# Optimization experiments

Hardware: AMD Instinct MI355X
Metric: run time of the kernel (lower is better)

## Reference

```python
import jax, jax.numpy as jnp
import numpy as np

B, T, V = 4096, 32, 256          # batch, decode steps, vocab
E, CE, H, L, NH = 768, 64, 256, 2, 4  # eword_dim, char_emb_dim, hidden, gru layers, heads
HD = H // NH                      # head dim
BOS, PAD = 1, 0


def _gru_cell(x, h, w_ih, w_hh, b_ih, b_hh):
    # PyTorch GRUCell math: gates ordered (r, z, n)
    gi = x @ w_ih.T + b_ih
    gh = h @ w_hh.T + b_hh
    ir, iz, inn = jnp.split(gi, 3, axis=-1)
    hr, hz, hn = jnp.split(gh, 3, axis=-1)
    r = jax.nn.sigmoid(ir + hr)
    z = jax.nn.sigmoid(iz + hz)
    n = jnp.tanh(inn + r * hn)
    return (1.0 - z) * n + z * h


def setup_inputs() -> dict:
    key = jax.random.key(0)
    ks = jax.random.split(key, 24)
    s = 0.02
    p = lambda k, shp: (jax.random.normal(k, shp, jnp.float32) * s)
    return {
        "eword": jax.random.normal(ks[0], (B, E), jnp.float32),
        "target_ids": jax.random.randint(ks[1], (B, T), 0, V),
        # params
        "char_emb": p(ks[2], (V, CE)).at[PAD].set(0.0),
        "eword_proj_w": p(ks[3], (H, E)), "eword_proj_b": p(ks[4], (H,)),
        "gru_w_ih0": p(ks[5], (3 * H, CE + E)), "gru_w_hh0": p(ks[6], (3 * H, H)),
        "gru_b_ih0": p(ks[7], (3 * H,)), "gru_b_hh0": p(ks[8], (3 * H,)),
        "gru_w_ih1": p(ks[9], (3 * H, H)), "gru_w_hh1": p(ks[10], (3 * H, H)),
        "gru_b_ih1": p(ks[11], (3 * H,)), "gru_b_hh1": p(ks[12], (3 * H,)),
        "attn_in_w": p(ks[13], (3 * H, H)), "attn_in_b": p(ks[14], (3 * H,)),
        "attn_out_w": p(ks[15], (H, H)), "attn_out_b": p(ks[16], (H,)),
        "key_w": p(ks[17], (H, E)), "key_b": p(ks[18], (H,)),
        "val_w": p(ks[19], (H, E)), "val_b": p(ks[20], (H,)),
        "proj_w": p(ks[21], (V, H)), "proj_b": p(ks[22], (V,)),
    }


def reference(eword, target_ids, char_emb, eword_proj_w, eword_proj_b,
              gru_w_ih0, gru_w_hh0, gru_b_ih0, gru_b_hh0,
              gru_w_ih1, gru_w_hh1, gru_b_ih1, gru_b_hh1,
              attn_in_w, attn_in_b, attn_out_w, attn_out_b,
              key_w, key_b, val_w, val_b, proj_w, proj_b):
    batch = eword.shape[0]
    # init hidden: tanh(Linear(eword)) broadcast across layers
    h0 = jnp.tanh(eword @ eword_proj_w.T + eword_proj_b)
    # pre-projected key/value (seq len 1), then MHA in-proj for k,v (static)
    wq, wk, wv = jnp.split(attn_in_w, 3, axis=0)
    bq, bk, bv = jnp.split(attn_in_b, 3)
    ek = (eword @ key_w.T + key_b) @ wk.T + bk        # (B, H)
    ev = (eword @ val_w.T + val_b) @ wv.T + bv        # (B, H)
    kh = ek.reshape(batch, NH, HD)                     # (B, NH, HD)
    vh = ev.reshape(batch, NH, HD)
    scale = 1.0 / np.sqrt(HD).astype(np.float32)

    # teacher forcing: input at step t is BOS for t=0, else target_ids[:, t-1]
    in_ids = jnp.concatenate(
        [jnp.full((batch, 1), BOS, target_ids.dtype), target_ids[:, :-1]], axis=1)

    def step(carry, ids):
        h_l0, h_l1 = carry
        ce = char_emb[ids] * (ids != PAD)[:, None].astype(char_emb.dtype)
        x = jnp.concatenate([ce, eword], axis=-1)     # (B, CE+E)
        h_l0 = _gru_cell(x, h_l0, gru_w_ih0, gru_w_hh0, gru_b_ih0, gru_b_hh0)
        h_l1 = _gru_cell(h_l0, h_l1, gru_w_ih1, gru_w_hh1, gru_b_ih1, gru_b_hh1)
        # single-query cross-attention over a length-1 key/value
        q = (h_l1 @ wq.T + bq).reshape(batch, NH, HD)
        score = jnp.sum(q * kh, axis=-1, keepdims=True) * scale  # (B, NH, 1)
        w = jax.nn.softmax(score, axis=-1)            # ones (len-1 softmax)
        attn = (w * vh).reshape(batch, H)
        attn_out = attn @ attn_out_w.T + attn_out_b
        out = h_l1 + attn_out
        logits = out @ proj_w.T + proj_b              # (B, V)
        return (h_l0, h_l1), logits

    _, logits_t = jax.lax.scan(step, (h0, h0), in_ids.T)  # (T, B, V)
    return jnp.transpose(logits_t, (1, 0, 2))              # (B, T, V)
```

## Files before the change

### kernel.cpp

```cpp
#include <hip/hip_runtime.h>


typedef __bf16 bf16;
typedef __attribute__((ext_vector_type(8))) __bf16 bf16x8;
typedef __attribute__((ext_vector_type(4))) __bf16 bf16x4;
typedef __attribute__((ext_vector_type(4))) float fx4;

#define MFMA16(a, b, c) __builtin_amdgcn_mfma_f32_16x16x32_bf16(a, b, c, 0, 0, 0)

__device__ __forceinline__ float sigm(float x) { return 1.0f / (1.0f + expf(-x)); }

__device__ __forceinline__ bf16x8 cvt8(const float* __restrict__ p) {
    float4 u = ((const float4*)p)[0];
    float4 v = ((const float4*)p)[1];
    bf16x8 r;
    r[0] = (bf16)u.x; r[1] = (bf16)u.y; r[2] = (bf16)u.z; r[3] = (bf16)u.w;
    r[4] = (bf16)v.x; r[5] = (bf16)v.y; r[6] = (bf16)v.z; r[7] = (bf16)v.w;
    return r;
}

__device__ __forceinline__ bf16x8 addcvt8(bf16x8 h, const float* __restrict__ p) {
    float4 u = ((const float4*)p)[0];
    float4 v = ((const float4*)p)[1];
    bf16x8 r;
    r[0] = (bf16)((float)h[0] + u.x); r[1] = (bf16)((float)h[1] + u.y);
    r[2] = (bf16)((float)h[2] + u.z); r[3] = (bf16)((float)h[3] + u.w);
    r[4] = (bf16)((float)h[4] + v.x); r[5] = (bf16)((float)h[5] + v.y);
    r[6] = (bf16)((float)h[6] + v.z); r[7] = (bf16)((float)h[7] + v.w);
    return r;
}

__global__ void f2b(const float* __restrict__ s, bf16* __restrict__ d, int n) {
    int i = (blockIdx.x * 256 + threadIdx.x) * 4;
    if (i >= n) return;
    float4 v = *(const float4*)(s + i);
    bf16x4 o;
    o[0] = (bf16)v.x; o[1] = (bf16)v.y; o[2] = (bf16)v.z; o[3] = (bf16)v.w;
    *(bf16x4*)(d + i) = o;
}

__global__ __launch_bounds__(256, 4) void gemm_bt(
    const float* __restrict__ A, int lda,
    const float* __restrict__ W, int ldw,
    const float* __restrict__ bias,
    float* __restrict__ out, int ldo, int act_tanh, int K)
{
    const int tid  = threadIdx.x;
    const int wid  = tid >> 6;
    const int lane = tid & 63;
    const int quad = lane >> 4;
    const int l16  = lane & 15;
    const int m0   = blockIdx.x * 32;
    const int n0   = blockIdx.y * 256 + wid * 64;

    fx4 acc[4][2];
#pragma unroll
    for (int j = 0; j < 4; ++j) {
        acc[j][0] = fx4{0.f, 0.f, 0.f, 0.f};
        acc[j][1] = fx4{0.f, 0.f, 0.f, 0.f};
    }

    const float* a0p = A + (size_t)(m0 + l16) * lda + quad * 8;
    const float* a1p = A + (size_t)(m0 + 16 + l16) * lda + quad * 8;

    for (int k0 = 0; k0 < K; k0 += 32) {
        bf16x8 a0 = cvt8(a0p + k0);
        bf16x8 a1 = cvt8(a1p + k0);
#pragma unroll
        for (int j = 0; j < 4; ++j) {
            bf16x8 b = cvt8(W + (size_t)(n0 + j * 16 + l16) * ldw + k0 + quad * 8);
            acc[j][0] = MFMA16(a0, b, acc[j][0]);
            acc[j][1] = MFMA16(a1, b, acc[j][1]);
        }
    }

#pragma unroll
    for (int j = 0; j < 4; ++j) {
        int n = n0 + j * 16 + l16;
        float bv = bias ? bias[n] : 0.0f;
#pragma unroll
        for (int rt = 0; rt < 2; ++rt)
#pragma unroll
            for (int r = 0; r < 4; ++r) {
                int m = m0 + rt * 16 + quad * 4 + r;
                float v = acc[j][rt][r] + bv;
                if (act_tanh) v = tanhf(v);
                out[(size_t)m * ldo + n] = v;
            }
    }
}

__global__ __launch_bounds__(1024, 4) void decoder_loop(
    const int*   __restrict__ tgt,
    const float* __restrict__ h0i,
    const float* __restrict__ gword,
    const float* __restrict__ cproj,
    const bf16*  __restrict__ w_hh0, const float* __restrict__ b_hh0,
    const bf16*  __restrict__ w_ih1, const float* __restrict__ b_ih1,
    const bf16*  __restrict__ w_hh1, const float* __restrict__ b_hh1,
    bf16* __restrict__ h1all)
{
    __shared__ __align__(16) bf16 hb0[2][16][264];
    __shared__ __align__(16) bf16 hb1[2][16][264];

    const int tid  = threadIdx.x;
    const int wid  = tid >> 6;
    const int lane = tid & 63;
    const int quad = lane >> 4;
    const int l16  = lane & 15;
    const int row0 = blockIdx.x * 16;
    const int col  = wid * 16 + l16;
    const int rw   = quad * 4;

    float h0m[4], h1m[4], cg[3][4];
    float bh0[3], bi1[3], bh1[3];
#pragma unroll
    for (int g = 0; g < 3; ++g) {
        bh0[g] = b_hh0[g * 256 + col];
        bi1[g] = b_ih1[g * 256 + col];
        bh1[g] = b_hh1[g * 256 + col];
    }
#pragma unroll
    for (int r = 0; r < 4; ++r) {
        int row = row0 + rw + r;
        float v = h0i[(size_t)row * 256 + col];
        h0m[r] = v; h1m[r] = v;
        bf16 bv = (bf16)v;
        hb0[0][rw + r][col] = bv; hb1[0][rw + r][col] = bv;
#pragma unroll
        for (int g = 0; g < 3; ++g)
            cg[g][r] = cproj[(size_t)768 + g * 256 + col]
                     + gword[(size_t)row * 768 + g * 256 + col];
    }

    const char* Wp0 = (const char*)w_hh0;
    const char* Wp1 = (const char*)w_ih1;
    const char* Wp2 = (const char*)w_hh1;
    int woff[3];
#pragma unroll
    for (int g = 0; g < 3; ++g)
        woff[g] = ((g * 256 + col) * 256 + quad * 8) * 2;

    __syncthreads();

    for (int t = 0; t < 32; ++t) {
        const int p = t & 1, q = p ^ 1;

        int nid[4];
#pragma unroll
        for (int r = 0; r < 4; ++r)
            nid[r] = tgt[(row0 + rw + r) * 32 + t];

        fx4 g0[3], g1[3];
#pragma unroll
        for (int g = 0; g < 3; ++g) {
            g0[g] = fx4{0.f, 0.f, 0.f, 0.f};
            g1[g] = fx4{0.f, 0.f, 0.f, 0.f};
        }
        bf16x8 av[2], cv[2], wb0[2], wb2[2];
        av[0] = *(const bf16x8*)&hb0[p][l16][quad * 8];
        cv[0] = *(const bf16x8*)&hb1[p][l16][quad * 8];
        av[1] = *(const bf16x8*)&hb0[p][l16][32 + quad * 8];
        cv[1] = *(const bf16x8*)&hb1[p][l16][32 + quad * 8];
        wb0[0] = *(const bf16x8*)(Wp0 + woff[0]);
        wb2[0] = *(const bf16x8*)(Wp2 + woff[0]);
        wb0[1] = *(const bf16x8*)(Wp0 + woff[1]);
        wb2[1] = *(const bf16x8*)(Wp2 + woff[1]);
#pragma unroll
        for (int kk = 0; kk < 8; ++kk) {
            bf16x8 au = av[kk & 1], cu = cv[kk & 1];
            if (kk < 6) {
                av[kk & 1] = *(const bf16x8*)&hb0[p][l16][(kk + 2) * 32 + quad * 8];
                cv[kk & 1] = *(const bf16x8*)&hb1[p][l16][(kk + 2) * 32 + quad * 8];
            }
#pragma unroll
            for (int g = 0; g < 3; ++g) {
                const int s = kk * 3 + g;
                bf16x8 b0 = wb0[s & 1], b2 = wb2[s & 1];
                if (s + 2 < 24) {
                    const int g2 = (s + 2) % 3, k2 = (s + 2) / 3;
                    wb0[s & 1] = *(const bf16x8*)(Wp0 + woff[g2] + k2 * 64);
                    wb2[s & 1] = *(const bf16x8*)(Wp2 + woff[g2] + k2 * 64);
                }
                g0[g] = MFMA16(au, b0, g0[g]);
                g1[g] = MFMA16(cu, b2, g1[g]);
            }
        }
#pragma unroll
        for (int r = 0; r < 4; ++r) {
            float rr = sigm(cg[0][r] + g0[0][r] + bh0[0]);
            float zz = sigm(cg[1][r] + g0[1][r] + bh0[1]);
            float nn = tanhf(cg[2][r] + rr * (g0[2][r] + bh0[2]));
            h0m[r] = (1.0f - zz) * nn + zz * h0m[r];
            hb0[q][rw + r][col] = (bf16)h0m[r];
        }
        __syncthreads();

        float cgn[3][4];
#pragma unroll
        for (int g = 0; g < 3; ++g)
#pragma unroll
            for (int r = 0; r < 4; ++r)
                cgn[g][r] = cproj[(size_t)nid[r] * 768 + g * 256 + col]
                          + gword[(size_t)(row0 + rw + r) * 768 + g * 256 + col];

        fx4 gi[3];
#pragma unroll
        for (int g = 0; g < 3; ++g) gi[g] = fx4{0.f, 0.f, 0.f, 0.f};
        bf16x8 bv2[2], wb1[2];
        bv2[0] = *(const bf16x8*)&hb0[q][l16][quad * 8];
        bv2[1] = *(const bf16x8*)&hb0[q][l16][32 + quad * 8];
        wb1[0] = *(const bf16x8*)(Wp1 + woff[0]);
        wb1[1] = *(const bf16x8*)(Wp1 + woff[1]);
#pragma unroll
        for (int kk = 0; kk < 8; ++kk) {
            bf16x8 au = bv2[kk & 1];
            if (kk < 6)
                bv2[kk & 1] = *(const bf16x8*)&hb0[q][l16][(kk + 2) * 32 + quad * 8];
#pragma unroll
            for (int g = 0; g < 3; ++g) {
                const int s = kk * 3 + g;
                bf16x8 b = wb1[s & 1];
                if (s + 2 < 24) {
                    const int g2 = (s + 2) % 3, k2 = (s + 2) / 3;
                    wb1[s & 1] = *(const bf16x8*)(Wp1 + woff[g2] + k2 * 64);
                }
                gi[g] = MFMA16(au, b, gi[g]);
            }
        }
#pragma unroll
        for (int r = 0; r < 4; ++r) {
            float rr = sigm(gi[0][r] + bi1[0] + g1[0][r] + bh1[0]);
            float zz = sigm(gi[1][r] + bi1[1] + g1[1][r] + bh1[1]);
            float nn = tanhf(gi[2][r] + bi1[2] + rr * (g1[2][r] + bh1[2]));
            h1m[r] = (1.0f - zz) * nn + zz * h1m[r];
            bf16 hv = (bf16)h1m[r];
            hb1[q][rw + r][col] = hv;
            __builtin_nontemporal_store(
                hv, &h1all[((size_t)(row0 + rw + r) * 32 + t) * 256 + col]);
        }
#pragma unroll
        for (int g = 0; g < 3; ++g)
#pragma unroll
            for (int r = 0; r < 4; ++r) cg[g][r] = cgn[g][r];

        __syncthreads();
    }
}

__global__ __launch_bounds__(256, 4) void logits_final(
    const bf16*  __restrict__ h1,
    const float* __restrict__ a2,
    const bf16*  __restrict__ pw,
    const float* __restrict__ pb,
    float* __restrict__ out)
{
    const int tid  = threadIdx.x;
    const int wid  = tid >> 6;
    const int lane = tid & 63;
    const int quad = lane >> 4;
    const int l16  = lane & 15;
    const int m0   = blockIdx.x * 32;
    const int n0   = wid * 64;
    const int b    = m0 >> 5;

    fx4 acc[4][2];
#pragma unroll
    for (int j = 0; j < 4; ++j) {
        acc[j][0] = fx4{0.f, 0.f, 0.f, 0.f};
        acc[j][1] = fx4{0.f, 0.f, 0.f, 0.f};
    }

    for (int k0 = 0; k0 < 256; k0 += 32) {
        bf16x8 h0 = *(const bf16x8*)(h1 + (size_t)(m0 + l16) * 256 + k0 + quad * 8);
        bf16x8 h1v = *(const bf16x8*)(h1 + (size_t)(m0 + 16 + l16) * 256 + k0 + quad * 8);
        const float* ap = a2 + (size_t)b * 256 + k0 + quad * 8;
        bf16x8 a0 = addcvt8(h0, ap);
        bf16x8 a1 = addcvt8(h1v, ap);
#pragma unroll
        for (int j = 0; j < 4; ++j) {
            bf16x8 bb = *(const bf16x8*)(pw + (size_t)(n0 + j * 16 + l16) * 256 + k0 + quad * 8);
            acc[j][0] = MFMA16(a0, bb, acc[j][0]);
            acc[j][1] = MFMA16(a1, bb, acc[j][1]);
        }
    }

#pragma unroll
    for (int j = 0; j < 4; ++j) {
        int n = n0 + j * 16 + l16;
        float bv = pb[n];
#pragma unroll
        for (int rt = 0; rt < 2; ++rt)
#pragma unroll
            for (int r = 0; r < 4; ++r) {
                int m = m0 + rt * 16 + quad * 4 + r;
                out[(size_t)m * 256 + n] = acc[j][rt][r] + bv;
            }
    }
}

extern "C" void kernel_launch(void* const* d_in, const int* in_sizes, int n_in,
                              void* d_out, int out_size, void* d_ws, size_t ws_size,
                              hipStream_t stream)
{
    const float* eword      = (const float*)d_in[0];
    const int*   tgt        = (const int*)  d_in[1];
    const float* char_emb   = (const float*)d_in[2];
    const float* ew_w       = (const float*)d_in[3];
    const float* ew_b       = (const float*)d_in[4];
    const float* w_ih0      = (const float*)d_in[5];
    const float* w_hh0      = (const float*)d_in[6];
    const float* b_ih0      = (const float*)d_in[7];
    const float* b_hh0      = (const float*)d_in[8];
    const float* w_ih1      = (const float*)d_in[9];
    const float* w_hh1      = (const float*)d_in[10];
    const float* b_ih1      = (const float*)d_in[11];
    const float* b_hh1      = (const float*)d_in[12];
    const float* attn_in_w  = (const float*)d_in[13];
    const float* attn_in_b  = (const float*)d_in[14];
    const float* attn_out_w = (const float*)d_in[15];
    const float* attn_out_b = (const float*)d_in[16];
    const float* val_w      = (const float*)d_in[19];
    const float* val_b      = (const float*)d_in[20];
    const float* proj_w     = (const float*)d_in[21];
    const float* proj_b     = (const float*)d_in[22];

    char* ws = (char*)d_ws;
    float* h0i   = (float*)ws;  ws += (size_t)4096 * 256 * 4;
    float* gwrd  = (float*)ws;  ws += (size_t)4096 * 768 * 4;
    float* cproj = (float*)ws;  ws += (size_t)256  * 768 * 4;
    float* a2    = (float*)ws;  ws += (size_t)4096 * 256 * 4;
    float* buf1  = (float*)ws;  ws += (size_t)4096 * 256 * 4;
    float* buf2  = (float*)ws;  ws += (size_t)4096 * 256 * 4;
    bf16*  wbhh0 = (bf16*)ws;   ws += (size_t)768 * 256 * 2;
    bf16*  wbih1 = (bf16*)ws;   ws += (size_t)768 * 256 * 2;
    bf16*  wbhh1 = (bf16*)ws;   ws += (size_t)768 * 256 * 2;
    bf16*  wbprj = (bf16*)ws;   ws += (size_t)256 * 256 * 2;
    bf16*  h1all = (bf16*)ws;   ws += (size_t)4096 * 32 * 256 * 2;

    dim3 blk(256);
    f2b<<<dim3(192), blk, 0, stream>>>(w_hh0, wbhh0, 768 * 256);
    f2b<<<dim3(192), blk, 0, stream>>>(w_ih1, wbih1, 768 * 256);
    f2b<<<dim3(192), blk, 0, stream>>>(w_hh1, wbhh1, 768 * 256);
    f2b<<<dim3(64),  blk, 0, stream>>>(proj_w, wbprj, 256 * 256);

    gemm_bt<<<dim3(128, 1), blk, 0, stream>>>(eword, 768, ew_w, 768, ew_b, h0i, 256, 1, 768);
    gemm_bt<<<dim3(128, 3), blk, 0, stream>>>(eword, 768, w_ih0 + 64, 832, b_ih0, gwrd, 768, 0, 768);
    gemm_bt<<<dim3(8, 3),   blk, 0, stream>>>(char_emb, 64, w_ih0, 832, nullptr, cproj, 768, 0, 64);
    gemm_bt<<<dim3(128, 1), blk, 0, stream>>>(eword, 768, val_w, 768, val_b, buf1, 256, 0, 768);
    gemm_bt<<<dim3(128, 1), blk, 0, stream>>>(buf1, 256, attn_in_w + 512 * 256, 256, attn_in_b + 512, buf2, 256, 0, 256);
    gemm_bt<<<dim3(128, 1), blk, 0, stream>>>(buf2, 256, attn_out_w, 256, attn_out_b, a2, 256, 0, 256);

    decoder_loop<<<dim3(256), dim3(1024), 0, stream>>>(
        tgt, h0i, gwrd, cproj,
        wbhh0, b_hh0, wbih1, b_ih1, wbhh1, b_hh1, h1all);

    logits_final<<<dim3(4096), blk, 0, stream>>>(h1all, a2, wbprj, proj_b, (float*)d_out);
}
```

Before: 2.263 ms.

## Pack GRU weights into per-wave MFMA fragment layout for coalesced loads

Adds a packing kernel that reorders the three bf16 GRU weight matrices so each wave's B-fragments for all gates and K-chunks are laid out contiguously. Each 16-lane group then reads 512 contiguous bytes per fragment instead of rows strided by 512 bytes. The decoder loop switches to a one-ahead prefetch of all three gate fragments per K-chunk and moves the target-id load to after the barrier. Register pressure may rise because six weight fragments are held in flight at once.

```diff
diff --git a/kernel.cpp b/kernel.cpp
--- a/kernel.cpp
+++ b/kernel.cpp
@@ -37,6 +37,17 @@
     bf16x4 o;
     o[0] = (bf16)v.x; o[1] = (bf16)v.y; o[2] = (bf16)v.z; o[3] = (bf16)v.w;
     *(bf16x4*)(d + i) = o;
+}
+
+__global__ void wpack(const float* __restrict__ src, bf16* __restrict__ dst) {
+    int gid = blockIdx.x * 256 + threadIdx.x;
+    if (gid >= 768 * 32) return;
+    int gc = gid >> 5, piece = gid & 31;
+    int g = gc >> 8, rem = gc & 255, w = rem >> 4, l16 = rem & 15;
+    int c = piece >> 2, quad = piece & 3;
+    bf16x8 v = cvt8(src + (size_t)gc * 256 + piece * 8);
+    size_t d = (size_t)w * 12288 + (size_t)(c * 3 + g) * 512 + l16 * 32 + quad * 8;
+    *(bf16x8*)(dst + d) = v;
 }
 
 __global__ __launch_bounds__(256, 4) void gemm_bt(
@@ -95,9 +106,9 @@
     const float* __restrict__ h0i,
     const float* __restrict__ gword,
     const float* __restrict__ cproj,
-    const bf16*  __restrict__ w_hh0, const float* __restrict__ b_hh0,
-    const bf16*  __restrict__ w_ih1, const float* __restrict__ b_ih1,
-    const bf16*  __restrict__ w_hh1, const float* __restrict__ b_hh1,
+    const bf16*  __restrict__ w_hh0p, const float* __restrict__ b_hh0,
+    const bf16*  __restrict__ w_ih1p, const float* __restrict__ b_ih1,
+    const bf16*  __restrict__ w_hh1p, const float* __restrict__ b_hh1,
     bf16* __restrict__ h1all)
 {
     __shared__ __align__(16) bf16 hb0[2][16][264];
@@ -112,6 +123,10 @@
     const int col  = wid * 16 + l16;
     const int rw   = quad * 4;
 
+    const bf16* pW0 = w_hh0p + (size_t)wid * 12288 + l16 * 32 + quad * 8;
+    const bf16* pW1 = w_ih1p + (size_t)wid * 12288 + l16 * 32 + quad * 8;
+    const bf16* pW2 = w_hh1p + (size_t)wid * 12288 + l16 * 32 + quad * 8;
+
     float h0m[4], h1m[4], cg[3][4];
     float bh0[3], bi1[3], bh1[3];
 #pragma unroll
@@ -133,23 +148,10 @@
                      + gword[(size_t)row * 768 + g * 256 + col];
     }
 
-    const char* Wp0 = (const char*)w_hh0;
-    const char* Wp1 = (const char*)w_ih1;
-    const char* Wp2 = (const char*)w_hh1;
-    int woff[3];
-#pragma unroll
-    for (int g = 0; g < 3; ++g)
-        woff[g] = ((g * 256 + col) * 256 + quad * 8) * 2;
-
     __syncthreads();
 
     for (int t = 0; t < 32; ++t) {
         const int p = t & 1, q = p ^ 1;
-
-        int nid[4];
-#pragma unroll
-        for (int r = 0; r < 4; ++r)
-            nid[r] = tgt[(row0 + rw + r) * 32 + t];
 
         fx4 g0[3], g1[3];
 #pragma unroll
@@ -157,33 +159,35 @@
             g0[g] = fx4{0.f, 0.f, 0.f, 0.f};
             g1[g] = fx4{0.f, 0.f, 0.f, 0.f};
         }
-        bf16x8 av[2], cv[2], wb0[2], wb2[2];
-        av[0] = *(const bf16x8*)&hb0[p][l16][quad * 8];
-        cv[0] = *(const bf16x8*)&hb1[p][l16][quad * 8];
-        av[1] = *(const bf16x8*)&hb0[p][l16][32 + quad * 8];
-        cv[1] = *(const bf16x8*)&hb1[p][l16][32 + quad * 8];
-        wb0[0] = *(const bf16x8*)(Wp0 + woff[0]);
-        wb2[0] = *(const bf16x8*)(Wp2 + woff[0]);
-        wb0[1] = *(const bf16x8*)(Wp0 + woff[1]);
-        wb2[1] = *(const bf16x8*)(Wp2 + woff[1]);
+        bf16x8 a_c, c_c, w0[3], w2[3];
+        a_c = *(const bf16x8*)&hb0[p][l16][quad * 8];
+        c_c = *(const bf16x8*)&hb1[p][l16][quad * 8];
+#pragma unroll
+        for (int g = 0; g < 3; ++g) {
+            w0[g] = *(const bf16x8*)(pW0 + g * 512);
+            w2[g] = *(const bf16x8*)(pW2 + g * 512);
+        }
 #pragma unroll
         for (int kk = 0; kk < 8; ++kk) {
-            bf16x8 au = av[kk & 1], cu = cv[kk & 1];
-            if (kk < 6) {
-                av[kk & 1] = *(const bf16x8*)&hb0[p][l16][(kk + 2) * 32 + quad * 8];
-                cv[kk & 1] = *(const bf16x8*)&hb1[p][l16][(kk + 2) * 32 + quad * 8];
+            bf16x8 a_n, c_n, w0n[3], w2n[3];
+            if (kk < 7) {
+                a_n = *(const bf16x8*)&hb0[p][l16][(kk + 1) * 32 + quad * 8];
+                c_n = *(const bf16x8*)&hb1[p][l16][(kk + 1) * 32 + quad * 8];
+#pragma unroll
+                for (int g = 0; g < 3; ++g) {
+                    w0n[g] = *(const bf16x8*)(pW0 + ((kk + 1) * 3 + g) * 512);
+                    w2n[g] = *(const bf16x8*)(pW2 + ((kk + 1) * 3 + g) * 512);
+                }
             }
 #pragma unroll
             for (int g = 0; g < 3; ++g) {
-                const int s = kk * 3 + g;
-                bf16x8 b0 = wb0[s & 1], b2 = wb2[s & 1];
-                if (s + 2 < 24) {
-                    const int g2 = (s + 2) % 3, k2 = (s + 2) / 3;
-                    wb0[s & 1] = *(const bf16x8*)(Wp0 + woff[g2] + k2 * 64);
-                    wb2[s & 1] = *(const bf16x8*)(Wp2 + woff[g2] + k2 * 64);
-                }
-                g0[g] = MFMA16(au, b0, g0[g]);
-                g1[g] = MFMA16(cu, b2, g1[g]);
+                g0[g] = MFMA16(a_c, w0[g], g0[g]);
+                g1[g] = MFMA16(c_c, w2[g], g1[g]);
+            }
+            if (kk < 7) {
+                a_c = a_n; c_c = c_n;
+#pragma unroll
+                for (int g = 0; g < 3; ++g) { w0[g] = w0n[g]; w2[g] = w2n[g]; }
             }
         }
 #pragma unroll
@@ -196,6 +200,10 @@
         }
         __syncthreads();
 
+        int nid[4];
+#pragma unroll
+        for (int r = 0; r < 4; ++r)
+            nid[r] = tgt[(row0 + rw + r) * 32 + t];
         float cgn[3][4];
 #pragma unroll
         for (int g = 0; g < 3; ++g)
@@ -207,25 +215,27 @@
         fx4 gi[3];
 #pragma unroll
         for (int g = 0; g < 3; ++g) gi[g] = fx4{0.f, 0.f, 0.f, 0.f};
-        bf16x8 bv2[2], wb1[2];
-        bv2[0] = *(const bf16x8*)&hb0[q][l16][quad * 8];
-        bv2[1] = *(const bf16x8*)&hb0[q][l16][32 + quad * 8];
-        wb1[0] = *(const bf16x8*)(Wp1 + woff[0]);
-        wb1[1] = *(const bf16x8*)(Wp1 + woff[1]);
+        bf16x8 b_c, w1[3];
+        b_c = *(const bf16x8*)&hb0[q][l16][quad * 8];
+#pragma unroll
+        for (int g = 0; g < 3; ++g)
+            w1[g] = *(const bf16x8*)(pW1 + g * 512);
 #pragma unroll
         for (int kk = 0; kk < 8; ++kk) {
-            bf16x8 au = bv2[kk & 1];
-            if (kk < 6)
-                bv2[kk & 1] = *(const bf16x8*)&hb0[q][l16][(kk + 2) * 32 + quad * 8];
-#pragma unroll
-            for (int g = 0; g < 3; ++g) {
-                const int s = kk * 3 + g;
-                bf16x8 b = wb1[s & 1];
-                if (s + 2 < 24) {
-                    const int g2 = (s + 2) % 3, k2 = (s + 2) / 3;
-                    wb1[s & 1] = *(const bf16x8*)(Wp1 + woff[g2] + k2 * 64);
-                }
-                gi[g] = MFMA16(au, b, gi[g]);
+            bf16x8 b_n, w1n[3];
+            if (kk < 7) {
+                b_n = *(const bf16x8*)&hb0[q][l16][(kk + 1) * 32 + quad * 8];
+#pragma unroll
+                for (int g = 0; g < 3; ++g)
+                    w1n[g] = *(const bf16x8*)(pW1 + ((kk + 1) * 3 + g) * 512);
+            }
+#pragma unroll
+            for (int g = 0; g < 3; ++g)
+                gi[g] = MFMA16(b_c, w1[g], gi[g]);
+            if (kk < 7) {
+                b_c = b_n;
+#pragma unroll
+                for (int g = 0; g < 3; ++g) w1[g] = w1n[g];
             }
         }
 #pragma unroll
@@ -339,9 +349,9 @@
     bf16*  h1all = (bf16*)ws;   ws += (size_t)4096 * 32 * 256 * 2;
 
     dim3 blk(256);
-    f2b<<<dim3(192), blk, 0, stream>>>(w_hh0, wbhh0, 768 * 256);
-    f2b<<<dim3(192), blk, 0, stream>>>(w_ih1, wbih1, 768 * 256);
-    f2b<<<dim3(192), blk, 0, stream>>>(w_hh1, wbhh1, 768 * 256);
+    wpack<<<dim3(96), blk, 0, stream>>>(w_hh0, wbhh0);
+    wpack<<<dim3(96), blk, 0, stream>>>(w_ih1, wbih1);
+    wpack<<<dim3(96), blk, 0, stream>>>(w_hh1, wbhh1);
     f2b<<<dim3(64),  blk, 0, stream>>>(proj_w, wbprj, 256 * 256);
 
     gemm_bt<<<dim3(128, 1), blk, 0, stream>>>(eword, 768, ew_w, 768, ew_b, h0i, 256, 1, 768);
```

Measured after the change: 2.236 ms. About the same (-1.2%).
